# Optimization experiments

Hardware: AMD Instinct MI355X
Metric: run time of the kernel (lower is better)

The kernel has to match this reference:

```python
import jax, jax.numpy as jnp
import numpy as np

NUM_HEADS = 12
WINDOW = 7            # window_size (and window_pretrain)
MASK_WINDOWS = 64     # windows per image (56x56 feature map / 7x7 windows)
TABLE_SIZE = (2 * WINDOW - 1) ** 2  # 169


def setup_inputs() -> dict:
    key = jax.random.key(0)
    ks = jax.random.split(key, 8)
    B, L, C = 2048, WINDOW * WINDOW, 384
    x = jax.random.normal(ks[0], (B, L, C), jnp.float32)
    rel_index = jax.random.randint(ks[1], (L * L,), 0, TABLE_SIZE, jnp.int32)
    attn_mask = jax.random.normal(ks[2], (1, MASK_WINDOWS, 1, L, L), jnp.float32) * 0.05
    # learned params
    qkv_w = jax.random.normal(ks[3], (C, 3 * C), jnp.float32) * 0.02
    qkv_b = jnp.zeros((3 * C,), jnp.float32)
    rel_bias_table = jax.random.normal(ks[4], (TABLE_SIZE, NUM_HEADS), jnp.float32) * 0.02
    proj_w = jax.random.normal(ks[5], (C, C), jnp.float32) * 0.02
    proj_b = jnp.zeros((C,), jnp.float32)
    return {"x": x, "rel_index": rel_index, "attn_mask": attn_mask,
            "qkv_w": qkv_w, "qkv_b": qkv_b, "rel_bias_table": rel_bias_table,
            "proj_w": proj_w, "proj_b": proj_b}


def reference(x, rel_index, attn_mask, qkv_w, qkv_b, rel_bias_table, proj_w, proj_b):
    B, L, C = x.shape
    H = NUM_HEADS
    D = C // H
    scale = D ** -0.5
    # qkv projection -> [3, B, H, L, D]
    qkv = (x @ qkv_w + qkv_b).reshape(B, L, 3, H, D).transpose(2, 0, 3, 1, 4)
    q, k, v = qkv[0], qkv[1], qkv[2]
    attn = jnp.einsum('bhqd,bhkd->bhqk', q * scale, k)  # [B,H,L,L]
    # gathered relative position bias: [L*L, H] -> [H, L, L]
    bias = rel_bias_table[rel_index].reshape(L, L, H).transpose(2, 0, 1)
    attn = attn + bias[None]
    # shifted-window mask add (with_mask=True path)
    attn = attn.reshape(-1, MASK_WINDOWS, H, L, L) + attn_mask
    attn = attn.reshape(-1, H, L, L)
    attn = jax.nn.softmax(attn, axis=-1)
    out = jnp.einsum('bhqk,bhkd->bqhd', attn, v).reshape(B, L, C)
    return out @ proj_w + proj_b
```

## Files before the change

kernel.cpp:

```cpp
#include <hip/hip_runtime.h>

typedef _Float16 half8 __attribute__((ext_vector_type(8)));
typedef float f32x4 __attribute__((ext_vector_type(4)));

constexpr int NB = 2048;
constexpr int CDIM = 384;
constexpr int NH = 12;
constexpr int MM = NB * 49;
constexpr int NTOT = 1152;
constexpr float SCALE = 0.17677669529663687f;

constexpr int XBLK = 37632;
constexpr int WBLK = 2304;

constexpr int QKV_BLOCKS = 9 * (MM / 128);
constexpr int QKV_CHUNK  = QKV_BLOCKS / 8;
constexpr int PROJ_BLOCKS = 3 * (MM / 128);
constexpr int PROJ_CHUNK  = PROJ_BLOCKS / 8;

__device__ __forceinline__ void async16(const void* g, void* l) {
    __builtin_amdgcn_global_load_lds((const __attribute__((address_space(1))) void*)g,
                                     (__attribute__((address_space(3))) void*)l, 16, 0, 0);
}


__global__ __launch_bounds__(256) void prep(const float* __restrict__ x,
                                            const float* __restrict__ qkv_w,
                                            const float* __restrict__ proj_w,
                                            const int* __restrict__ rel_index,
                                            const float* __restrict__ rtable,
                                            const float* __restrict__ mask,
                                            _Float16* __restrict__ x_h,
                                            _Float16* __restrict__ qkvT,
                                            _Float16* __restrict__ projT,
                                            float* __restrict__ FT) {
    int bid = blockIdx.x;
    if (bid < XBLK) {
        size_t i = ((size_t)bid * 256 + threadIdx.x) * 4;
        float4 v = *(const float4*)(x + i);
        _Float16 h0 = (_Float16)v.x, h1 = (_Float16)v.y, h2 = (_Float16)v.z, h3 = (_Float16)v.w;
        _Float16* o = x_h + i;
        o[0] = h0; o[1] = h1; o[2] = h2; o[3] = h3;
    } else if (bid < XBLK + WBLK) {
        int i = (bid - XBLK) * 256 + threadIdx.x;
        if (i < 1152 * 384) {
            int n = i / 384, kk = i % 384;
            qkvT[i] = (_Float16)qkv_w[kk * 1152 + n];
        } else {
            int j = i - 1152 * 384;
            int n = j / 384, kk = j % 384;
            projT[j] = (_Float16)proj_w[kk * 384 + n];
        }
    } else {
        int wh = bid - XBLK - WBLK;
        int w = wh / 12, h = wh - w * 12;
        float* dst = FT + (size_t)wh * 4096;
        for (int idx = threadIdx.x; idx < 4096; idx += 256) {
            int k = idx >> 6, q = idx & 63;
            float v = 0.f;
            if (k < 49 && q < 49)
                v = rtable[rel_index[q * 49 + k] * NH + h] + mask[(size_t)w * 2401 + q * 49 + k];
            dst[idx] = v;
        }
    }
}


__global__ __launch_bounds__(256) void gemm_qkv(const _Float16* __restrict__ A,
                                                const _Float16* __restrict__ Bt,
                                                const float* __restrict__ qkv_b,
                                                _Float16* __restrict__ C) {
    __shared__ union {
        struct { _Float16 A[128 * 64]; _Float16 B[128 * 64]; } st;
        _Float16 tile[64 * 136];
    } sm;
    _Float16* As = sm.st.A;
    _Float16* Bs = sm.st.B;

    const int K = 384;
    const int bid = blockIdx.x;
    const int wid = (bid & 7) * QKV_CHUNK + (bid >> 3);
    const int tn = wid % 9, tm = wid / 9;
    const int t = threadIdx.x;
    const int wave = t >> 6, lane = t & 63;
    const int wm = (wave & 1) * 64, wn = (wave >> 1) * 64;
    const int quad = lane >> 4, l16 = lane & 15;
    const int rsub = lane >> 3, p = lane & 7;

    f32x4 acc[4][4] = {};
    const _Float16* Abase = A + (size_t)(tm * 128) * K;
    const _Float16* Bbase = Bt + (size_t)(tn * 128) * K;

    for (int k0 = 0; k0 < K; k0 += 64) {
        __syncthreads();
#pragma unroll
        for (int n = 0; n < 4; n++) {
            int ni = wave * 4 + n;
            int row = ni * 8 + rsub;
            int chunk = p ^ (row & 7);
            async16(Abase + (size_t)row * K + k0 + chunk * 8, (char*)As + ni * 1024);
            async16(Bbase + (size_t)row * K + k0 + chunk * 8, (char*)Bs + ni * 1024);
        }
        __syncthreads();
#pragma unroll
        for (int ks = 0; ks < 2; ks++) {
            half8 af[4], bfv[4];
#pragma unroll
            for (int i = 0; i < 4; i++)
                af[i] = *(const half8*)(&As[(wm + i * 16 + l16) * 64 + (((ks * 4 + quad) ^ (l16 & 7)) * 8)]);
#pragma unroll
            for (int j = 0; j < 4; j++)
                bfv[j] = *(const half8*)(&Bs[(wn + j * 16 + l16) * 64 + (((ks * 4 + quad) ^ (l16 & 7)) * 8)]);
#pragma unroll
            for (int i = 0; i < 4; i++)
#pragma unroll
                for (int j = 0; j < 4; j++)
                    acc[i][j] = __builtin_amdgcn_mfma_f32_16x16x32_f16(af[i], bfv[j], acc[i][j], 0, 0, 0);
        }
    }

    __syncthreads();
    const int nbase = tn * 128, mbase = tm * 128;
    const float s = (tn < 3) ? SCALE : 1.f;
    float bj[4];
#pragma unroll
    for (int j = 0; j < 4; j++) bj[j] = qkv_b[nbase + wn + j * 16 + l16];

    const int rcol = (t & 15) * 8;
    const int rrow0 = t >> 4;

    for (int h = 0; h < 2; h++) {
        if ((wave & 1) == h) {
#pragma unroll
            for (int j = 0; j < 4; j++) {
                int n = wn + j * 16 + l16;
#pragma unroll
                for (int i = 0; i < 4; i++) {
#pragma unroll
                    for (int r = 0; r < 4; r++) {
                        int m = i * 16 + quad * 4 + r;
                        sm.tile[m * 136 + n] = (_Float16)((acc[i][j][r] + bj[j]) * s);
                    }
                }
            }
        }
        __syncthreads();
#pragma unroll
        for (int g = 0; g < 4; g++) {
            int row = g * 16 + rrow0;
            half8 val = *(const half8*)(&sm.tile[row * 136 + rcol]);
            *(half8*)(C + (size_t)(mbase + h * 64 + row) * NTOT + nbase + rcol) = val;
        }
        __syncthreads();
    }
}


__global__ __launch_bounds__(256) void attn_kernel(const _Float16* __restrict__ C,
                                                   const float* __restrict__ FT,
                                                   _Float16* __restrict__ out) {
    __shared__ _Float16 Vt[4][32 * 72];
    __shared__ _Float16 Pb[4][16 * 72];
    const int t = threadIdx.x;
    const int wave = t >> 6, lane = t & 63, quad = lane >> 4, l16 = lane & 15;
    const int gw = blockIdx.x * 4 + wave;
    const int b = gw / 12, h = gw - b * 12;

    const _Float16* qb = C + (size_t)b * 49 * NTOT + h * 32;
    const _Float16* kb = qb + 384;
    const _Float16* vb = qb + 768;
    const float* Fb = FT + ((size_t)((b & 63) * 12 + h)) * 4096;

    _Float16* vt = Vt[wave];
    {
        int d = lane >> 1, seg = lane & 1;
        half8 z = {};
        *(half8*)(&vt[d * 72 + 48 + seg * 8]) = z;
    }
#pragma unroll
    for (int i2 = 0; i2 < 4; i2++) {
        int l = i2 * 16 + (lane >> 2);
        int d0 = (lane & 3) * 8;
        if (l < 49) {
            half8 v8 = *(const half8*)(vb + (size_t)l * NTOT + d0);
#pragma unroll
            for (int e = 0; e < 8; e++)
                vt[(d0 + e) * 72 + l] = v8[e];
        }
    }

    half8 bk[4];
#pragma unroll
    for (int j = 0; j < 4; j++) {
        int krow = j * 16 + l16; if (krow > 48) krow = 48;
        bk[j] = *(const half8*)(kb + (size_t)krow * NTOT + quad * 8);
    }
    half8 bv[2][2];
#pragma unroll
    for (int nt = 0; nt < 2; nt++)
#pragma unroll
        for (int ks = 0; ks < 2; ks++)
            bv[nt][ks] = *(const half8*)(&vt[(nt * 16 + l16) * 72 + ks * 32 + quad * 8]);

    _Float16* Pw = Pb[wave];
#pragma unroll
    for (int i = 0; i < 4; i++) {
        int qrow = i * 16 + l16; if (qrow > 48) qrow = 48;
        half8 aq = *(const half8*)(qb + (size_t)qrow * NTOT + quad * 8);

        f32x4 acc[4];
#pragma unroll
        for (int j = 0; j < 4; j++)
            acc[j] = *(const f32x4*)(Fb + (j * 16 + l16) * 64 + i * 16 + quad * 4);
#pragma unroll
        for (int j = 0; j < 4; j++)
            acc[j] = __builtin_amdgcn_mfma_f32_16x16x32_f16(aq, bk[j], acc[j], 0, 0, 0);

        if (l16 != 0) {
#pragma unroll
            for (int r = 0; r < 4; r++) acc[3][r] = -1e30f;
        }

        float rinv[4];
#pragma unroll
        for (int r = 0; r < 4; r++) {
            float m = fmaxf(fmaxf(acc[0][r], acc[1][r]), fmaxf(acc[2][r], acc[3][r]));
            m = fmaxf(m, __shfl_xor(m, 1, 64));
            m = fmaxf(m, __shfl_xor(m, 2, 64));
            m = fmaxf(m, __shfl_xor(m, 4, 64));
            m = fmaxf(m, __shfl_xor(m, 8, 64));
            float sum = 0.f;
#pragma unroll
            for (int j = 0; j < 4; j++) {
                float e = __expf(acc[j][r] - m);
                acc[j][r] = e;
                sum += e;
            }
            sum += __shfl_xor(sum, 1, 64);
            sum += __shfl_xor(sum, 2, 64);
            sum += __shfl_xor(sum, 4, 64);
            sum += __shfl_xor(sum, 8, 64);
            rinv[r] = 1.f / sum;
        }

#pragma unroll
        for (int j = 0; j < 4; j++)
#pragma unroll
            for (int r = 0; r < 4; r++)
                Pw[(quad * 4 + r) * 72 + j * 16 + l16] = (_Float16)acc[j][r];

        f32x4 oacc[2] = {};
#pragma unroll
        for (int ks = 0; ks < 2; ks++) {
            half8 ap = *(const half8*)(&Pw[l16 * 72 + ks * 32 + quad * 8]);
#pragma unroll
            for (int nt = 0; nt < 2; nt++)
                oacc[nt] = __builtin_amdgcn_mfma_f32_16x16x32_f16(ap, bv[nt][ks], oacc[nt], 0, 0, 0);
        }

#pragma unroll
        for (int nt = 0; nt < 2; nt++)
#pragma unroll
            for (int r = 0; r < 4; r++) {
                int q = i * 16 + quad * 4 + r;
                if (q < 49)
                    out[((size_t)b * 49 + q) * CDIM + h * 32 + nt * 16 + l16] =
                        (_Float16)(oacc[nt][r] * rinv[r]);
            }
    }
}


__global__ __launch_bounds__(256) void gemm_proj(const _Float16* __restrict__ A,
                                                 const _Float16* __restrict__ Bt,
                                                 const float* __restrict__ proj_b,
                                                 float* __restrict__ out) {
    __shared__ _Float16 As[128 * 64];
    __shared__ _Float16 Bs[128 * 64];
    const int K = 384;
    const int bid = blockIdx.x;
    const int wid = (bid & 7) * PROJ_CHUNK + (bid >> 3);
    const int tn = wid % 3, tm = wid / 3;
    const int t = threadIdx.x;
    const int wave = t >> 6, lane = t & 63;
    const int wm = (wave & 1) * 64, wn = (wave >> 1) * 64;
    const int quad = lane >> 4, l16 = lane & 15;
    const int rsub = lane >> 3, p = lane & 7;

    f32x4 acc[4][4] = {};
    const _Float16* Abase = A + (size_t)(tm * 128) * K;
    const _Float16* Bbase = Bt + (size_t)(tn * 128) * K;

    for (int k0 = 0; k0 < K; k0 += 64) {
        __syncthreads();
#pragma unroll
        for (int n = 0; n < 4; n++) {
            int ni = wave * 4 + n;
            int row = ni * 8 + rsub;
            int chunk = p ^ (row & 7);
            async16(Abase + (size_t)row * K + k0 + chunk * 8, (char*)As + ni * 1024);
            async16(Bbase + (size_t)row * K + k0 + chunk * 8, (char*)Bs + ni * 1024);
        }
        __syncthreads();
#pragma unroll
        for (int ks = 0; ks < 2; ks++) {
            half8 af[4], bfv[4];
#pragma unroll
            for (int i = 0; i < 4; i++)
                af[i] = *(const half8*)(&As[(wm + i * 16 + l16) * 64 + (((ks * 4 + quad) ^ (l16 & 7)) * 8)]);
#pragma unroll
            for (int j = 0; j < 4; j++)
                bfv[j] = *(const half8*)(&Bs[(wn + j * 16 + l16) * 64 + (((ks * 4 + quad) ^ (l16 & 7)) * 8)]);
#pragma unroll
            for (int i = 0; i < 4; i++)
#pragma unroll
                for (int j = 0; j < 4; j++)
                    acc[i][j] = __builtin_amdgcn_mfma_f32_16x16x32_f16(af[i], bfv[j], acc[i][j], 0, 0, 0);
        }
    }

    const int mbase = tm * 128, nbase = tn * 128;
#pragma unroll
    for (int j = 0; j < 4; j++) {
        int n = nbase + wn + j * 16 + l16;
        float bias = proj_b[n];
#pragma unroll
        for (int i = 0; i < 4; i++) {
#pragma unroll
            for (int r = 0; r < 4; r++) {
                int m = mbase + wm + i * 16 + quad * 4 + r;
                out[(size_t)m * CDIM + n] = acc[i][j][r] + bias;
            }
        }
    }
}


extern "C" void kernel_launch(void* const* d_in, const int* in_sizes, int n_in,
                              void* d_out, int out_size, void* d_ws, size_t ws_size,
                              hipStream_t stream) {
    const float* x        = (const float*)d_in[0];
    const int*   rel_idx  = (const int*)d_in[1];
    const float* amask    = (const float*)d_in[2];
    const float* qkv_w    = (const float*)d_in[3];
    const float* qkv_b    = (const float*)d_in[4];
    const float* rtable   = (const float*)d_in[5];
    const float* proj_w   = (const float*)d_in[6];
    const float* proj_b   = (const float*)d_in[7];
    float* out = (float*)d_out;

    char* w = (char*)d_ws;
    const size_t XB = (size_t)MM * CDIM * 2;
    const size_t CB = (size_t)MM * NTOT * 2;
    _Float16* x_h    = (_Float16*)w;
    _Float16* wqkvT  = (_Float16*)(w + XB);
    _Float16* wprojT = (_Float16*)(w + XB + 884736);
    _Float16* Cbuf   = (_Float16*)(w + XB + 884736 + 294912);
    float*    FT     = (float*)(w + XB + 884736 + 294912 + CB);
    _Float16* ao_h   = x_h;

    prep<<<XBLK + WBLK + 768, 256, 0, stream>>>(x, qkv_w, proj_w, rel_idx, rtable, amask,
                                                x_h, wqkvT, wprojT, FT);
    gemm_qkv<<<QKV_BLOCKS, 256, 0, stream>>>(x_h, wqkvT, qkv_b, Cbuf);
    attn_kernel<<<NB * NH / 4, 256, 0, stream>>>(Cbuf, FT, ao_h);
    gemm_proj<<<PROJ_BLOCKS, 256, 0, stream>>>(ao_h, wprojT, proj_b, out);
}
```

Baseline: 632.6 us.

## Restructure QKV and projection GEMMs to 64-row tiles with full-K LDS and register-resident weights

Both GEMMs now use 64x128 output tiles with 512 threads. Each block loads its whole 64x384 A slab into LDS in one pass, and each wave keeps its 16 columns of weights in registers across all of K. This removes the per-K-step double barrier loop and the repeated B loads into LDS. The projection output is now staged through LDS so it can be written with coalesced float4 stores. In exchange, each wave does less MFMA work per A fragment read, grids are twice as large, and LDS use per block rises to 48KB, which may reduce occupancy.

```diff
diff --git a/kernel.cpp b/kernel.cpp
--- a/kernel.cpp
+++ b/kernel.cpp
@@ -13,9 +13,9 @@
 constexpr int XBLK = 37632;
 constexpr int WBLK = 2304;
 
-constexpr int QKV_BLOCKS = 9 * (MM / 128);
+constexpr int QKV_BLOCKS = 9 * (MM / 64);
 constexpr int QKV_CHUNK  = QKV_BLOCKS / 8;
-constexpr int PROJ_BLOCKS = 3 * (MM / 128);
+constexpr int PROJ_BLOCKS = 3 * (MM / 64);
 constexpr int PROJ_CHUNK  = PROJ_BLOCKS / 8;
 
 __device__ __forceinline__ void async16(const void* g, void* l) {
@@ -66,92 +66,71 @@
 }
 
 
-__global__ __launch_bounds__(256) void gemm_qkv(const _Float16* __restrict__ A,
+__global__ __launch_bounds__(512) void gemm_qkv(const _Float16* __restrict__ A,
                                                 const _Float16* __restrict__ Bt,
                                                 const float* __restrict__ qkv_b,
                                                 _Float16* __restrict__ C) {
     __shared__ union {
-        struct { _Float16 A[128 * 64]; _Float16 B[128 * 64]; } st;
+        _Float16 As[64 * 384];
         _Float16 tile[64 * 136];
     } sm;
-    _Float16* As = sm.st.A;
-    _Float16* Bs = sm.st.B;
-
     const int K = 384;
     const int bid = blockIdx.x;
     const int wid = (bid & 7) * QKV_CHUNK + (bid >> 3);
     const int tn = wid % 9, tm = wid / 9;
     const int t = threadIdx.x;
     const int wave = t >> 6, lane = t & 63;
-    const int wm = (wave & 1) * 64, wn = (wave >> 1) * 64;
     const int quad = lane >> 4, l16 = lane & 15;
-    const int rsub = lane >> 3, p = lane & 7;
-
-    f32x4 acc[4][4] = {};
-    const _Float16* Abase = A + (size_t)(tm * 128) * K;
-    const _Float16* Bbase = Bt + (size_t)(tn * 128) * K;
-
-    for (int k0 = 0; k0 < K; k0 += 64) {
-        __syncthreads();
-#pragma unroll
-        for (int n = 0; n < 4; n++) {
-            int ni = wave * 4 + n;
-            int row = ni * 8 + rsub;
-            int chunk = p ^ (row & 7);
-            async16(Abase + (size_t)row * K + k0 + chunk * 8, (char*)As + ni * 1024);
-            async16(Bbase + (size_t)row * K + k0 + chunk * 8, (char*)Bs + ni * 1024);
-        }
-        __syncthreads();
-#pragma unroll
-        for (int ks = 0; ks < 2; ks++) {
-            half8 af[4], bfv[4];
-#pragma unroll
-            for (int i = 0; i < 4; i++)
-                af[i] = *(const half8*)(&As[(wm + i * 16 + l16) * 64 + (((ks * 4 + quad) ^ (l16 & 7)) * 8)]);
-#pragma unroll
-            for (int j = 0; j < 4; j++)
-                bfv[j] = *(const half8*)(&Bs[(wn + j * 16 + l16) * 64 + (((ks * 4 + quad) ^ (l16 & 7)) * 8)]);
-#pragma unroll
-            for (int i = 0; i < 4; i++)
-#pragma unroll
-                for (int j = 0; j < 4; j++)
-                    acc[i][j] = __builtin_amdgcn_mfma_f32_16x16x32_f16(af[i], bfv[j], acc[i][j], 0, 0, 0);
-        }
-    }
-
-    __syncthreads();
-    const int nbase = tn * 128, mbase = tm * 128;
+
+    const _Float16* Abase = A + (size_t)(tm * 64) * K;
+#pragma unroll
+    for (int rnd = 0; rnd < 6; rnd++) {
+        int f = rnd * 512 + t;
+        int row = f / 48, pos = f - row * 48;
+        int c = (pos & ~7) | ((pos & 7) ^ (row & 7));
+        async16(Abase + (size_t)row * K + c * 8, (char*)sm.As + (rnd * 8192 + wave * 1024));
+    }
+
+    const int nbase = tn * 128;
+    const int myn = wave * 16 + l16;
+    const _Float16* Bb = Bt + (size_t)(nbase + myn) * K + quad * 8;
+    half8 breg[12];
+#pragma unroll
+    for (int kk = 0; kk < 12; kk++) breg[kk] = *(const half8*)(Bb + kk * 32);
+
+    __syncthreads();
+
+    f32x4 acc[4] = {};
+#pragma unroll
+    for (int kk = 0; kk < 12; kk++) {
+#pragma unroll
+        for (int i = 0; i < 4; i++) {
+            int row = i * 16 + l16;
+            int c = kk * 4 + quad;
+            int pos = (c & ~7) | ((c & 7) ^ (row & 7));
+            half8 a = *(const half8*)(&sm.As[row * 384 + pos * 8]);
+            acc[i] = __builtin_amdgcn_mfma_f32_16x16x32_f16(a, breg[kk], acc[i], 0, 0, 0);
+        }
+    }
+
+    const int mbase = tm * 64;
     const float s = (tn < 3) ? SCALE : 1.f;
-    float bj[4];
-#pragma unroll
-    for (int j = 0; j < 4; j++) bj[j] = qkv_b[nbase + wn + j * 16 + l16];
-
-    const int rcol = (t & 15) * 8;
-    const int rrow0 = t >> 4;
-
-    for (int h = 0; h < 2; h++) {
-        if ((wave & 1) == h) {
-#pragma unroll
-            for (int j = 0; j < 4; j++) {
-                int n = wn + j * 16 + l16;
-#pragma unroll
-                for (int i = 0; i < 4; i++) {
-#pragma unroll
-                    for (int r = 0; r < 4; r++) {
-                        int m = i * 16 + quad * 4 + r;
-                        sm.tile[m * 136 + n] = (_Float16)((acc[i][j][r] + bj[j]) * s);
-                    }
-                }
-            }
-        }
-        __syncthreads();
-#pragma unroll
-        for (int g = 0; g < 4; g++) {
-            int row = g * 16 + rrow0;
-            half8 val = *(const half8*)(&sm.tile[row * 136 + rcol]);
-            *(half8*)(C + (size_t)(mbase + h * 64 + row) * NTOT + nbase + rcol) = val;
-        }
-        __syncthreads();
+    const float bb = qkv_b[nbase + myn];
+    __syncthreads();
+#pragma unroll
+    for (int i = 0; i < 4; i++)
+#pragma unroll
+        for (int r = 0; r < 4; r++) {
+            int m = i * 16 + quad * 4 + r;
+            sm.tile[m * 136 + myn] = (_Float16)((acc[i][r] + bb) * s);
+        }
+    __syncthreads();
+#pragma unroll
+    for (int g = 0; g < 2; g++) {
+        int idx = g * 512 + t;
+        int row = idx >> 4, c8 = idx & 15;
+        half8 val = *(const half8*)(&sm.tile[row * 136 + c8 * 8]);
+        *(half8*)(C + (size_t)(mbase + row) * NTOT + nbase + c8 * 8) = val;
     }
 }
 
@@ -271,67 +250,70 @@
 }
 
 
-__global__ __launch_bounds__(256) void gemm_proj(const _Float16* __restrict__ A,
+__global__ __launch_bounds__(512) void gemm_proj(const _Float16* __restrict__ A,
                                                  const _Float16* __restrict__ Bt,
                                                  const float* __restrict__ proj_b,
                                                  float* __restrict__ out) {
-    __shared__ _Float16 As[128 * 64];
-    __shared__ _Float16 Bs[128 * 64];
+    __shared__ union {
+        _Float16 As[64 * 384];
+        float tilef[64 * 132];
+    } sm;
     const int K = 384;
     const int bid = blockIdx.x;
     const int wid = (bid & 7) * PROJ_CHUNK + (bid >> 3);
     const int tn = wid % 3, tm = wid / 3;
     const int t = threadIdx.x;
     const int wave = t >> 6, lane = t & 63;
-    const int wm = (wave & 1) * 64, wn = (wave >> 1) * 64;
     const int quad = lane >> 4, l16 = lane & 15;
-    const int rsub = lane >> 3, p = lane & 7;
-
-    f32x4 acc[4][4] = {};
-    const _Float16* Abase = A + (size_t)(tm * 128) * K;
-    const _Float16* Bbase = Bt + (size_t)(tn * 128) * K;
-
-    for (int k0 = 0; k0 < K; k0 += 64) {
-        __syncthreads();
-#pragma unroll
-        for (int n = 0; n < 4; n++) {
-            int ni = wave * 4 + n;
-            int row = ni * 8 + rsub;
-            int chunk = p ^ (row & 7);
-            async16(Abase + (size_t)row * K + k0 + chunk * 8, (char*)As + ni * 1024);
-            async16(Bbase + (size_t)row * K + k0 + chunk * 8, (char*)Bs + ni * 1024);
-        }
-        __syncthreads();
-#pragma unroll
-        for (int ks = 0; ks < 2; ks++) {
-            half8 af[4], bfv[4];
-#pragma unroll
-            for (int i = 0; i < 4; i++)
-                af[i] = *(const half8*)(&As[(wm + i * 16 + l16) * 64 + (((ks * 4 + quad) ^ (l16 & 7)) * 8)]);
-#pragma unroll
-            for (int j = 0; j < 4; j++)
-                bfv[j] = *(const half8*)(&Bs[(wn + j * 16 + l16) * 64 + (((ks * 4 + quad) ^ (l16 & 7)) * 8)]);
-#pragma unroll
-            for (int i = 0; i < 4; i++)
-#pragma unroll
-                for (int j = 0; j < 4; j++)
-                    acc[i][j] = __builtin_amdgcn_mfma_f32_16x16x32_f16(af[i], bfv[j], acc[i][j], 0, 0, 0);
-        }
-    }
-
-    const int mbase = tm * 128, nbase = tn * 128;
-#pragma unroll
-    for (int j = 0; j < 4; j++) {
-        int n = nbase + wn + j * 16 + l16;
-        float bias = proj_b[n];
+
+    const _Float16* Abase = A + (size_t)(tm * 64) * K;
+#pragma unroll
+    for (int rnd = 0; rnd < 6; rnd++) {
+        int f = rnd * 512 + t;
+        int row = f / 48, pos = f - row * 48;
+        int c = (pos & ~7) | ((pos & 7) ^ (row & 7));
+        async16(Abase + (size_t)row * K + c * 8, (char*)sm.As + (rnd * 8192 + wave * 1024));
+    }
+
+    const int nbase = tn * 128;
+    const int myn = wave * 16 + l16;
+    const _Float16* Bb = Bt + (size_t)(nbase + myn) * K + quad * 8;
+    half8 breg[12];
+#pragma unroll
+    for (int kk = 0; kk < 12; kk++) breg[kk] = *(const half8*)(Bb + kk * 32);
+
+    __syncthreads();
+
+    f32x4 acc[4] = {};
+#pragma unroll
+    for (int kk = 0; kk < 12; kk++) {
 #pragma unroll
         for (int i = 0; i < 4; i++) {
-#pragma unroll
-            for (int r = 0; r < 4; r++) {
-                int m = mbase + wm + i * 16 + quad * 4 + r;
-                out[(size_t)m * CDIM + n] = acc[i][j][r] + bias;
-            }
-        }
+            int row = i * 16 + l16;
+            int c = kk * 4 + quad;
+            int pos = (c & ~7) | ((c & 7) ^ (row & 7));
+            half8 a = *(const half8*)(&sm.As[row * 384 + pos * 8]);
+            acc[i] = __builtin_amdgcn_mfma_f32_16x16x32_f16(a, breg[kk], acc[i], 0, 0, 0);
+        }
+    }
+
+    const int mbase = tm * 64;
+    const float bb = proj_b[nbase + myn];
+    __syncthreads();
+#pragma unroll
+    for (int i = 0; i < 4; i++)
+#pragma unroll
+        for (int r = 0; r < 4; r++) {
+            int m = i * 16 + quad * 4 + r;
+            sm.tilef[m * 132 + myn] = acc[i][r] + bb;
+        }
+    __syncthreads();
+#pragma unroll
+    for (int g = 0; g < 4; g++) {
+        int idx = g * 512 + t;
+        int row = idx >> 5, c4 = idx & 31;
+        float4 val = *(const float4*)(&sm.tilef[row * 132 + c4 * 4]);
+        *(float4*)(out + (size_t)(mbase + row) * CDIM + nbase + c4 * 4) = val;
     }
 }
 
@@ -361,7 +343,7 @@
 
     prep<<<XBLK + WBLK + 768, 256, 0, stream>>>(x, qkv_w, proj_w, rel_idx, rtable, amask,
                                                 x_h, wqkvT, wprojT, FT);
-    gemm_qkv<<<QKV_BLOCKS, 256, 0, stream>>>(x_h, wqkvT, qkv_b, Cbuf);
+    gemm_qkv<<<QKV_BLOCKS, 512, 0, stream>>>(x_h, wqkvT, qkv_b, Cbuf);
     attn_kernel<<<NB * NH / 4, 256, 0, stream>>>(Cbuf, FT, ao_h);
-    gemm_proj<<<PROJ_BLOCKS, 256, 0, stream>>>(ao_h, wprojT, proj_b, out);
-}
+    gemm_proj<<<PROJ_BLOCKS, 512, 0, stream>>>(ao_h, wprojT, proj_b, out);
+}
```

Result: slower. 708.6 us (+12.0%).

## Use 256x128 GEMM tiles with 512 threads and store bias/mask table in fp16

Applied to the files above, without the earlier changes.

Both GEMMs move from 128x128 tiles with 4 waves to 256x128 tiles with 8 waves, so each B tile loaded into LDS serves twice as many rows and fewer blocks are launched. The QKV epilogue is restructured into two passes that use two LDS staging tiles. The precomputed bias+mask table is stored in fp16 instead of fp32, halving its memory traffic in the attention kernel; it is now added after the MFMA rather than used as the accumulator's initial value. This costs some precision in the bias/mask and raises LDS use per block, which may lower occupancy.

```diff
diff --git a/kernel.cpp b/kernel.cpp
--- a/kernel.cpp
+++ b/kernel.cpp
@@ -1,6 +1,7 @@
 #include <hip/hip_runtime.h>
 
 typedef _Float16 half8 __attribute__((ext_vector_type(8)));
+typedef _Float16 half4 __attribute__((ext_vector_type(4)));
 typedef float f32x4 __attribute__((ext_vector_type(4)));
 
 constexpr int NB = 2048;
@@ -13,9 +14,9 @@
 constexpr int XBLK = 37632;
 constexpr int WBLK = 2304;
 
-constexpr int QKV_BLOCKS = 9 * (MM / 128);
+constexpr int QKV_BLOCKS = 9 * (MM / 256);
 constexpr int QKV_CHUNK  = QKV_BLOCKS / 8;
-constexpr int PROJ_BLOCKS = 3 * (MM / 128);
+constexpr int PROJ_BLOCKS = 3 * (MM / 256);
 constexpr int PROJ_CHUNK  = PROJ_BLOCKS / 8;
 
 __device__ __forceinline__ void async16(const void* g, void* l) {
@@ -33,7 +34,7 @@
                                             _Float16* __restrict__ x_h,
                                             _Float16* __restrict__ qkvT,
                                             _Float16* __restrict__ projT,
-                                            float* __restrict__ FT) {
+                                            _Float16* __restrict__ FTh) {
     int bid = blockIdx.x;
     if (bid < XBLK) {
         size_t i = ((size_t)bid * 256 + threadIdx.x) * 4;
@@ -54,25 +55,25 @@
     } else {
         int wh = bid - XBLK - WBLK;
         int w = wh / 12, h = wh - w * 12;
-        float* dst = FT + (size_t)wh * 4096;
+        _Float16* dst = FTh + (size_t)wh * 4096;
         for (int idx = threadIdx.x; idx < 4096; idx += 256) {
             int k = idx >> 6, q = idx & 63;
             float v = 0.f;
             if (k < 49 && q < 49)
                 v = rtable[rel_index[q * 49 + k] * NH + h] + mask[(size_t)w * 2401 + q * 49 + k];
-            dst[idx] = v;
-        }
-    }
-}
-
-
-__global__ __launch_bounds__(256) void gemm_qkv(const _Float16* __restrict__ A,
+            dst[idx] = (_Float16)v;
+        }
+    }
+}
+
+
+__global__ __launch_bounds__(512) void gemm_qkv(const _Float16* __restrict__ A,
                                                 const _Float16* __restrict__ Bt,
                                                 const float* __restrict__ qkv_b,
                                                 _Float16* __restrict__ C) {
     __shared__ union {
-        struct { _Float16 A[128 * 64]; _Float16 B[128 * 64]; } st;
-        _Float16 tile[64 * 136];
+        struct { _Float16 A[256 * 64]; _Float16 B[128 * 64]; } st;
+        _Float16 tile[2][64 * 136];
     } sm;
     _Float16* As = sm.st.A;
     _Float16* Bs = sm.st.B;
@@ -83,12 +84,12 @@
     const int tn = wid % 9, tm = wid / 9;
     const int t = threadIdx.x;
     const int wave = t >> 6, lane = t & 63;
-    const int wm = (wave & 1) * 64, wn = (wave >> 1) * 64;
+    const int wm = (wave & 3) * 64, wn = (wave >> 2) * 64;
     const int quad = lane >> 4, l16 = lane & 15;
     const int rsub = lane >> 3, p = lane & 7;
 
     f32x4 acc[4][4] = {};
-    const _Float16* Abase = A + (size_t)(tm * 128) * K;
+    const _Float16* Abase = A + (size_t)(tm * 256) * K;
     const _Float16* Bbase = Bt + (size_t)(tn * 128) * K;
 
     for (int k0 = 0; k0 < K; k0 += 64) {
@@ -99,6 +100,12 @@
             int row = ni * 8 + rsub;
             int chunk = p ^ (row & 7);
             async16(Abase + (size_t)row * K + k0 + chunk * 8, (char*)As + ni * 1024);
+        }
+#pragma unroll
+        for (int n = 0; n < 2; n++) {
+            int ni = wave * 2 + n;
+            int row = ni * 8 + rsub;
+            int chunk = p ^ (row & 7);
             async16(Bbase + (size_t)row * K + k0 + chunk * 8, (char*)Bs + ni * 1024);
         }
         __syncthreads();
@@ -119,45 +126,44 @@
         }
     }
 
-    __syncthreads();
-    const int nbase = tn * 128, mbase = tm * 128;
+    const int nbase = tn * 128, mbase = tm * 256;
     const float s = (tn < 3) ? SCALE : 1.f;
     float bj[4];
 #pragma unroll
     for (int j = 0; j < 4; j++) bj[j] = qkv_b[nbase + wn + j * 16 + l16];
 
-    const int rcol = (t & 15) * 8;
-    const int rrow0 = t >> 4;
-
-    for (int h = 0; h < 2; h++) {
-        if ((wave & 1) == h) {
+    for (int pass = 0; pass < 2; pass++) {
+        __syncthreads();
+        int hsel = (wave & 3) - pass * 2;
+        if (hsel == 0 || hsel == 1) {
+            _Float16* tl = sm.tile[hsel];
 #pragma unroll
             for (int j = 0; j < 4; j++) {
                 int n = wn + j * 16 + l16;
 #pragma unroll
-                for (int i = 0; i < 4; i++) {
+                for (int i = 0; i < 4; i++)
 #pragma unroll
                     for (int r = 0; r < 4; r++) {
                         int m = i * 16 + quad * 4 + r;
-                        sm.tile[m * 136 + n] = (_Float16)((acc[i][j][r] + bj[j]) * s);
+                        tl[m * 136 + n] = (_Float16)((acc[i][j][r] + bj[j]) * s);
                     }
-                }
             }
         }
         __syncthreads();
 #pragma unroll
         for (int g = 0; g < 4; g++) {
-            int row = g * 16 + rrow0;
-            half8 val = *(const half8*)(&sm.tile[row * 136 + rcol]);
-            *(half8*)(C + (size_t)(mbase + h * 64 + row) * NTOT + nbase + rcol) = val;
-        }
-        __syncthreads();
+            int idx = g * 512 + t;
+            int half = idx >> 10, rem = idx & 1023;
+            int row = rem >> 4, c8 = rem & 15;
+            half8 val = *(const half8*)(&sm.tile[half][row * 136 + c8 * 8]);
+            *(half8*)(C + (size_t)(mbase + (pass * 2 + half) * 64 + row) * NTOT + nbase + c8 * 8) = val;
+        }
     }
 }
 
 
 __global__ __launch_bounds__(256) void attn_kernel(const _Float16* __restrict__ C,
-                                                   const float* __restrict__ FT,
+                                                   const _Float16* __restrict__ FTh,
                                                    _Float16* __restrict__ out) {
     __shared__ _Float16 Vt[4][32 * 72];
     __shared__ _Float16 Pb[4][16 * 72];
@@ -169,7 +175,7 @@
     const _Float16* qb = C + (size_t)b * 49 * NTOT + h * 32;
     const _Float16* kb = qb + 384;
     const _Float16* vb = qb + 768;
-    const float* Fb = FT + ((size_t)((b & 63) * 12 + h)) * 4096;
+    const _Float16* Fb = FTh + ((size_t)((b & 63) * 12 + h)) * 4096;
 
     _Float16* vt = Vt[wave];
     {
@@ -208,13 +214,16 @@
         int qrow = i * 16 + l16; if (qrow > 48) qrow = 48;
         half8 aq = *(const half8*)(qb + (size_t)qrow * NTOT + quad * 8);
 
-        f32x4 acc[4];
-#pragma unroll
-        for (int j = 0; j < 4; j++)
-            acc[j] = *(const f32x4*)(Fb + (j * 16 + l16) * 64 + i * 16 + quad * 4);
+        f32x4 acc[4] = {};
 #pragma unroll
         for (int j = 0; j < 4; j++)
             acc[j] = __builtin_amdgcn_mfma_f32_16x16x32_f16(aq, bk[j], acc[j], 0, 0, 0);
+#pragma unroll
+        for (int j = 0; j < 4; j++) {
+            half4 fh = *(const half4*)(Fb + (j * 16 + l16) * 64 + i * 16 + quad * 4);
+#pragma unroll
+            for (int r = 0; r < 4; r++) acc[j][r] += (float)fh[r];
+        }
 
         if (l16 != 0) {
 #pragma unroll
@@ -271,11 +280,11 @@
 }
 
 
-__global__ __launch_bounds__(256) void gemm_proj(const _Float16* __restrict__ A,
+__global__ __launch_bounds__(512) void gemm_proj(const _Float16* __restrict__ A,
                                                  const _Float16* __restrict__ Bt,
                                                  const float* __restrict__ proj_b,
                                                  float* __restrict__ out) {
-    __shared__ _Float16 As[128 * 64];
+    __shared__ _Float16 As[256 * 64];
     __shared__ _Float16 Bs[128 * 64];
     const int K = 384;
     const int bid = blockIdx.x;
@@ -283,12 +292,12 @@
     const int tn = wid % 3, tm = wid / 3;
     const int t = threadIdx.x;
     const int wave = t >> 6, lane = t & 63;
-    const int wm = (wave & 1) * 64, wn = (wave >> 1) * 64;
+    const int wm = (wave & 3) * 64, wn = (wave >> 2) * 64;
     const int quad = lane >> 4, l16 = lane & 15;
     const int rsub = lane >> 3, p = lane & 7;
 
     f32x4 acc[4][4] = {};
-    const _Float16* Abase = A + (size_t)(tm * 128) * K;
+    const _Float16* Abase = A + (size_t)(tm * 256) * K;
     const _Float16* Bbase = Bt + (size_t)(tn * 128) * K;
 
     for (int k0 = 0; k0 < K; k0 += 64) {
@@ -299,6 +308,12 @@
             int row = ni * 8 + rsub;
             int chunk = p ^ (row & 7);
             async16(Abase + (size_t)row * K + k0 + chunk * 8, (char*)As + ni * 1024);
+        }
+#pragma unroll
+        for (int n = 0; n < 2; n++) {
+            int ni = wave * 2 + n;
+            int row = ni * 8 + rsub;
+            int chunk = p ^ (row & 7);
             async16(Bbase + (size_t)row * K + k0 + chunk * 8, (char*)Bs + ni * 1024);
         }
         __syncthreads();
@@ -319,7 +334,7 @@
         }
     }
 
-    const int mbase = tm * 128, nbase = tn * 128;
+    const int mbase = tm * 256, nbase = tn * 128;
 #pragma unroll
     for (int j = 0; j < 4; j++) {
         int n = nbase + wn + j * 16 + l16;
@@ -356,12 +371,12 @@
     _Float16* wqkvT  = (_Float16*)(w + XB);
     _Float16* wprojT = (_Float16*)(w + XB + 884736);
     _Float16* Cbuf   = (_Float16*)(w + XB + 884736 + 294912);
-    float*    FT     = (float*)(w + XB + 884736 + 294912 + CB);
+    _Float16* FTh    = (_Float16*)(w + XB + 884736 + 294912 + CB);
     _Float16* ao_h   = x_h;
 
     prep<<<XBLK + WBLK + 768, 256, 0, stream>>>(x, qkv_w, proj_w, rel_idx, rtable, amask,
-                                                x_h, wqkvT, wprojT, FT);
-    gemm_qkv<<<QKV_BLOCKS, 256, 0, stream>>>(x_h, wqkvT, qkv_b, Cbuf);
-    attn_kernel<<<NB * NH / 4, 256, 0, stream>>>(Cbuf, FT, ao_h);
-    gemm_proj<<<PROJ_BLOCKS, 256, 0, stream>>>(ao_h, wprojT, proj_b, out);
-}
+                                                x_h, wqkvT, wprojT, FTh);
+    gemm_qkv<<<QKV_BLOCKS, 512, 0, stream>>>(x_h, wqkvT, qkv_b, Cbuf);
+    attn_kernel<<<NB * NH / 4, 256, 0, stream>>>(Cbuf, FTh, ao_h);
+    gemm_proj<<<PROJ_BLOCKS, 512, 0, stream>>>(ao_h, wprojT, proj_b, out);
+}
```

Result: slower. 654.7 us (+3.5%).
